# Optimization experiments

Hardware: AMD Instinct MI355X
Metric: run time of the kernel (lower is better)

Reference implementation:

```python
import jax, jax.numpy as jnp
import numpy as np

BINS = 10


def setup_inputs() -> dict:
    key = jax.random.key(0)
    k1, k2 = jax.random.split(key)
    N = 16777216
    x = jax.random.normal(k1, (N, 1), dtype=jnp.float32)
    target = jax.random.randint(k2, (N,), 0, 2, dtype=jnp.int32)
    return {"x": x, "target": target}


def reference(x, target):
    # GHMC_Loss forward (binary, num_classes=1), first call (_last_bin_count is None).
    N = x.shape[0]
    logits = x[:, 0]                                   # [N]
    t = target.astype(x.dtype)                         # [N]

    # gradient norm g = |sigmoid(x) - t|  (detached in original)
    g = jnp.abs(jax.nn.sigmoid(logits) - t)            # [N]
    bin_idx = jnp.clip(
        jnp.floor(g * (BINS - 0.0001)).astype(jnp.int32), 0, BINS - 1
    )                                                  # [N]

    # single-pass histogram via scatter-add
    bin_count = jnp.zeros((BINS,), x.dtype).at[bin_idx].add(1.0)
    nonempty = (bin_count > 0).sum().astype(x.dtype)
    gd = jnp.maximum(bin_count * nonempty, 1e-6)
    beta = jnp.asarray(N, x.dtype) / gd                # [BINS]
    weights = beta[bin_idx]                            # [N] gather

    # stable BCE with logits: logaddexp(0, x) - x*t
    ce = jnp.logaddexp(jnp.zeros_like(logits), logits) - logits * t
    return jnp.mean(ce * weights)
```

## Files before the change

kernel.cpp:

```cpp
#include <hip/hip_runtime.h>

#define BINS 10
#define TPB 256
#define VEC_ITERS 16

__global__ __launch_bounds__(64) void ghmc_zero(float* ws) {
    if (threadIdx.x < 2 * BINS) ws[threadIdx.x] = 0.0f;
}

__device__ __forceinline__ void ghmc_accum(float z, int t, float2* acc, int tid) {
    float tf = (float)t;
    float az = fabsf(z);
    float e  = __expf(-az);
    float q  = 1.0f + e;
    float r  = __builtin_amdgcn_rcpf(q);
    float s  = (z >= 0.0f) ? r : e * r;
    float g  = fabsf(s - tf);
    int bin  = (int)(g * 9.9999f);
    bin = bin < (BINS - 1) ? bin : (BINS - 1);
    float ce = fmaxf(z, 0.0f) - z * tf + __logf(q);
    int i = bin * TPB + tid;
    float2 v = acc[i];
    v.x += ce;
    v.y += 1.0f;
    acc[i] = v;
}

__global__ __launch_bounds__(TPB) void ghmc_main(const float* __restrict__ x,
                                                 const int* __restrict__ tgt,
                                                 float* __restrict__ gsum,
                                                 float* __restrict__ gcnt,
                                                 int nvec, int ntotal) {
    __shared__ float2 acc[BINS * TPB];
    const int tid = threadIdx.x;
    #pragma unroll
    for (int b = 0; b < BINS; ++b) acc[b * TPB + tid] = make_float2(0.0f, 0.0f);

    const float4* __restrict__ x4 = (const float4*)x;
    const int4*  __restrict__ t4 = (const int4*)tgt;
    const int base = blockIdx.x * (TPB * VEC_ITERS) + tid;

    #pragma unroll 4
    for (int j = 0; j < VEC_ITERS; ++j) {
        int gi = base + j * TPB;
        if (gi < nvec) {
            float4 xv = x4[gi];
            int4   tv = t4[gi];
            ghmc_accum(xv.x, tv.x, acc, tid);
            ghmc_accum(xv.y, tv.y, acc, tid);
            ghmc_accum(xv.z, tv.z, acc, tid);
            ghmc_accum(xv.w, tv.w, acc, tid);
        }
    }
    if (blockIdx.x == 0) {
        for (int i = nvec * 4 + tid; i < ntotal; i += TPB) {
            ghmc_accum(x[i], tgt[i], acc, tid);
        }
    }

    __syncthreads();
    for (int sft = TPB / 2; sft > 0; sft >>= 1) {
        if (tid < sft) {
            #pragma unroll
            for (int b = 0; b < BINS; ++b) {
                float2 a = acc[b * TPB + tid];
                float2 o = acc[b * TPB + tid + sft];
                a.x += o.x;
                a.y += o.y;
                acc[b * TPB + tid] = a;
            }
        }
        __syncthreads();
    }
    if (tid < BINS) {
        atomicAdd(&gsum[tid], acc[tid * TPB].x);
        atomicAdd(&gcnt[tid], acc[tid * TPB].y);
    }
}

__global__ __launch_bounds__(64) void ghmc_final(const float* __restrict__ gsum,
                                                 const float* __restrict__ gcnt,
                                                 float* __restrict__ out) {
    int t = threadIdx.x;
    float cnt = (t < BINS) ? gcnt[t] : 0.0f;
    float sum = (t < BINS) ? gsum[t] : 0.0f;
    float ne  = (cnt > 0.0f) ? 1.0f : 0.0f;
    #pragma unroll
    for (int o = 32; o > 0; o >>= 1) ne += __shfl_down(ne, o);
    ne = __shfl(ne, 0);
    float term = (t < BINS) ? sum / fmaxf(cnt * ne, 1e-6f) : 0.0f;
    #pragma unroll
    for (int o = 32; o > 0; o >>= 1) term += __shfl_down(term, o);
    if (t == 0) out[0] = term;
}

extern "C" void kernel_launch(void* const* d_in, const int* in_sizes, int n_in,
                              void* d_out, int out_size, void* d_ws, size_t ws_size,
                              hipStream_t stream) {
    const float* x   = (const float*)d_in[0];
    const int*   tgt = (const int*)d_in[1];
    float* out  = (float*)d_out;
    float* gsum = (float*)d_ws;
    float* gcnt = gsum + BINS;

    int N    = in_sizes[0];
    int nvec = N / 4;
    int blocks = (nvec + TPB * VEC_ITERS - 1) / (TPB * VEC_ITERS);
    if (blocks < 1) blocks = 1;

    ghmc_zero<<<1, 64, 0, stream>>>(gsum);
    ghmc_main<<<blocks, TPB, 0, stream>>>(x, tgt, gsum, gcnt, nvec, N);
    ghmc_final<<<1, 64, 0, stream>>>(gsum, gcnt, out);
}
```

Measured before the change: 167.9 us.

## Replace global atomics with per-block partials and use LDS atomic adds

The zero-init kernel and the global atomicAdd merge are removed. Each block now writes its per-bin sums and counts to a partial buffer, and a 256-thread final kernel reduces those partials and computes the loss. Per-thread LDS accumulation switches from float2 read-modify-write to two separate arrays updated with LDS atomicAdd, and VEC_ITERS is halved with full unrolling. This saves a launch and the global atomic contention, and shortens the per-sample LDS dependency chain. In exchange it doubles the block count and needs a larger workspace (20 × nblocks floats).

Measured after the change: 322.9 us. 92.4% more time.

```diff
diff --git a/kernel.cpp b/kernel.cpp
--- a/kernel.cpp
+++ b/kernel.cpp
@@ -2,13 +2,10 @@
 
 #define BINS 10
 #define TPB 256
-#define VEC_ITERS 16
+#define VEC_ITERS 8
 
-__global__ __launch_bounds__(64) void ghmc_zero(float* ws) {
-    if (threadIdx.x < 2 * BINS) ws[threadIdx.x] = 0.0f;
-}
-
-__device__ __forceinline__ void ghmc_accum(float z, int t, float2* acc, int tid) {
+__device__ __forceinline__ void ghmc_accum(float z, int t,
+                                           float* lsum, float* lcnt, int tid) {
     float tf = (float)t;
     float az = fabsf(z);
     float e  = __expf(-az);
@@ -19,42 +16,42 @@
     int bin  = (int)(g * 9.9999f);
     bin = bin < (BINS - 1) ? bin : (BINS - 1);
     float ce = fmaxf(z, 0.0f) - z * tf + __logf(q);
-    int i = bin * TPB + tid;
-    float2 v = acc[i];
-    v.x += ce;
-    v.y += 1.0f;
-    acc[i] = v;
+    atomicAdd(&lsum[bin * TPB + tid], ce);
+    atomicAdd(&lcnt[bin * TPB + tid], 1.0f);
 }
 
 __global__ __launch_bounds__(TPB) void ghmc_main(const float* __restrict__ x,
                                                  const int* __restrict__ tgt,
-                                                 float* __restrict__ gsum,
-                                                 float* __restrict__ gcnt,
-                                                 int nvec, int ntotal) {
-    __shared__ float2 acc[BINS * TPB];
+                                                 float* __restrict__ part,
+                                                 int nvec, int ntotal, int nblocks) {
+    __shared__ float lsum[BINS * TPB];
+    __shared__ float lcnt[BINS * TPB];
     const int tid = threadIdx.x;
     #pragma unroll
-    for (int b = 0; b < BINS; ++b) acc[b * TPB + tid] = make_float2(0.0f, 0.0f);
+    for (int b = 0; b < BINS; ++b) {
+        lsum[b * TPB + tid] = 0.0f;
+        lcnt[b * TPB + tid] = 0.0f;
+    }
 
     const float4* __restrict__ x4 = (const float4*)x;
-    const int4*  __restrict__ t4 = (const int4*)tgt;
+    const int4*   __restrict__ t4 = (const int4*)tgt;
     const int base = blockIdx.x * (TPB * VEC_ITERS) + tid;
 
-    #pragma unroll 4
+    #pragma unroll
     for (int j = 0; j < VEC_ITERS; ++j) {
         int gi = base + j * TPB;
         if (gi < nvec) {
             float4 xv = x4[gi];
             int4   tv = t4[gi];
-            ghmc_accum(xv.x, tv.x, acc, tid);
-            ghmc_accum(xv.y, tv.y, acc, tid);
-            ghmc_accum(xv.z, tv.z, acc, tid);
-            ghmc_accum(xv.w, tv.w, acc, tid);
+            ghmc_accum(xv.x, tv.x, lsum, lcnt, tid);
+            ghmc_accum(xv.y, tv.y, lsum, lcnt, tid);
+            ghmc_accum(xv.z, tv.z, lsum, lcnt, tid);
+            ghmc_accum(xv.w, tv.w, lsum, lcnt, tid);
         }
     }
     if (blockIdx.x == 0) {
         for (int i = nvec * 4 + tid; i < ntotal; i += TPB) {
-            ghmc_accum(x[i], tgt[i], acc, tid);
+            ghmc_accum(x[i], tgt[i], lsum, lcnt, tid);
         }
     }
 
@@ -63,35 +60,48 @@
         if (tid < sft) {
             #pragma unroll
             for (int b = 0; b < BINS; ++b) {
-                float2 a = acc[b * TPB + tid];
-                float2 o = acc[b * TPB + tid + sft];
-                a.x += o.x;
-                a.y += o.y;
-                acc[b * TPB + tid] = a;
+                lsum[b * TPB + tid] += lsum[b * TPB + tid + sft];
+                lcnt[b * TPB + tid] += lcnt[b * TPB + tid + sft];
             }
         }
         __syncthreads();
     }
     if (tid < BINS) {
-        atomicAdd(&gsum[tid], acc[tid * TPB].x);
-        atomicAdd(&gcnt[tid], acc[tid * TPB].y);
+        part[tid * nblocks + blockIdx.x]          = lsum[tid * TPB];
+        part[(BINS + tid) * nblocks + blockIdx.x] = lcnt[tid * TPB];
     }
 }
 
-__global__ __launch_bounds__(64) void ghmc_final(const float* __restrict__ gsum,
-                                                 const float* __restrict__ gcnt,
-                                                 float* __restrict__ out) {
-    int t = threadIdx.x;
-    float cnt = (t < BINS) ? gcnt[t] : 0.0f;
-    float sum = (t < BINS) ? gsum[t] : 0.0f;
-    float ne  = (cnt > 0.0f) ? 1.0f : 0.0f;
+__global__ __launch_bounds__(TPB) void ghmc_final(const float* __restrict__ part,
+                                                  float* __restrict__ out, int nblocks) {
+    __shared__ float red[2 * BINS * TPB];
+    const int tid = threadIdx.x;
     #pragma unroll
-    for (int o = 32; o > 0; o >>= 1) ne += __shfl_down(ne, o);
-    ne = __shfl(ne, 0);
-    float term = (t < BINS) ? sum / fmaxf(cnt * ne, 1e-6f) : 0.0f;
-    #pragma unroll
-    for (int o = 32; o > 0; o >>= 1) term += __shfl_down(term, o);
-    if (t == 0) out[0] = term;
+    for (int s = 0; s < 2 * BINS; ++s) {
+        float v = 0.0f;
+        for (int i = tid; i < nblocks; i += TPB) v += part[s * nblocks + i];
+        red[s * TPB + tid] = v;
+    }
+    __syncthreads();
+    for (int sft = TPB / 2; sft > 0; sft >>= 1) {
+        if (tid < sft) {
+            #pragma unroll
+            for (int s = 0; s < 2 * BINS; ++s)
+                red[s * TPB + tid] += red[s * TPB + tid + sft];
+        }
+        __syncthreads();
+    }
+    if (tid == 0) {
+        float ne = 0.0f;
+        #pragma unroll
+        for (int b = 0; b < BINS; ++b)
+            ne += (red[(BINS + b) * TPB] > 0.0f) ? 1.0f : 0.0f;
+        float res = 0.0f;
+        #pragma unroll
+        for (int b = 0; b < BINS; ++b)
+            res += red[b * TPB] / fmaxf(red[(BINS + b) * TPB] * ne, 1e-6f);
+        out[0] = res;
+    }
 }
 
 extern "C" void kernel_launch(void* const* d_in, const int* in_sizes, int n_in,
@@ -100,15 +110,13 @@
     const float* x   = (const float*)d_in[0];
     const int*   tgt = (const int*)d_in[1];
     float* out  = (float*)d_out;
-    float* gsum = (float*)d_ws;
-    float* gcnt = gsum + BINS;
+    float* part = (float*)d_ws;
 
     int N    = in_sizes[0];
     int nvec = N / 4;
-    int blocks = (nvec + TPB * VEC_ITERS - 1) / (TPB * VEC_ITERS);
-    if (blocks < 1) blocks = 1;
+    int nblocks = (nvec + TPB * VEC_ITERS - 1) / (TPB * VEC_ITERS);
+    if (nblocks < 1) nblocks = 1;
 
-    ghmc_zero<<<1, 64, 0, stream>>>(gsum);
-    ghmc_main<<<blocks, TPB, 0, stream>>>(x, tgt, gsum, gcnt, nvec, N);
-    ghmc_final<<<1, 64, 0, stream>>>(gsum, gcnt, out);
+    ghmc_main<<<nblocks, TPB, 0, stream>>>(x, tgt, part, nvec, N, nblocks);
+    ghmc_final<<<1, TPB, 0, stream>>>(part, out, nblocks);
 }
```
